# Kernel optimization log

Measured on AMD Instinct MI355X. Metric: run time of the kernel, lower is better.

The kernel has to match this reference:

```python
import jax, jax.numpy as jnp
import numpy as np

N_NODES = 50000
N_EDGES = 600000
HID = 128


def setup_inputs() -> dict:
    key = jax.random.key(0)
    ks = jax.random.split(key, 10)
    s = 1.0 / np.sqrt(HID)
    s2 = 1.0 / np.sqrt(2 * HID)
    return {
        "h": jax.random.normal(ks[0], (N_NODES, HID), dtype=jnp.float32),
        "edge_index": jax.random.randint(ks[1], (2, N_EDGES), 0, N_NODES, dtype=jnp.int64),
        # edge_mlp: Linear(HID,HID) -> ReLU -> Linear(HID,HID); weights stored [in,out]
        "e_w1": jax.random.uniform(ks[2], (HID, HID), jnp.float32, -s, s),
        "e_b1": jax.random.uniform(ks[3], (HID,), jnp.float32, -s, s),
        "e_w2": jax.random.uniform(ks[4], (HID, HID), jnp.float32, -s, s),
        "e_b2": jax.random.uniform(ks[5], (HID,), jnp.float32, -s, s),
        # node_mlp: Linear(2*HID,HID) -> ReLU -> Linear(HID,HID)
        "n_w1": jax.random.uniform(ks[6], (2 * HID, HID), jnp.float32, -s2, s2),
        "n_b1": jax.random.uniform(ks[7], (HID,), jnp.float32, -s2, s2),
        "n_w2": jax.random.uniform(ks[8], (HID, HID), jnp.float32, -s, s),
        "n_b2": jax.random.uniform(ks[9], (HID,), jnp.float32, -s, s),
    }


def reference(h, edge_index, e_w1, e_b1, e_w2, e_b2, n_w1, n_b1, n_w2, n_b2):
    row, col = edge_index[0], edge_index[1]
    # edge model: MLP(h[row] - h[col])  [E, HID]
    diff = h[row] - h[col]
    e = jax.nn.relu(diff @ e_w1 + e_b1) @ e_w2 + e_b2
    # aggregate messages to source nodes (unsorted_segment_sum over row)
    agg = jax.ops.segment_sum(e, row, num_segments=h.shape[0])  # [N, HID]
    # node model: MLP(concat(h, agg))
    z = jnp.concatenate([h, agg], axis=1)  # [N, 2*HID]
    out = jax.nn.relu(z @ n_w1 + n_b1) @ n_w2 + n_b2
    return out
```

## Files before the change

### kernel.cpp

```cpp
#include <hip/hip_runtime.h>
#include <hip/hip_bf16.h>


typedef __attribute__((ext_vector_type(4))) float f32x4;
typedef __attribute__((ext_vector_type(2))) float f32x2;
typedef __attribute__((ext_vector_type(8))) __bf16 bf16x8;
typedef __attribute__((ext_vector_type(4))) short s16x4;
typedef __attribute__((ext_vector_type(8))) unsigned short u16x8;

#define SLOT_CAP 64

__device__ __forceinline__ short f2bf(float f) {
  unsigned x = __float_as_uint(f);
  x = (x + 0x7fffu + ((x >> 16) & 1u)) >> 16;
  return (short)x;
}
__device__ __forceinline__ float bf2f(unsigned short u) {
  return __uint_as_float(((unsigned)u) << 16);
}
__device__ __forceinline__ int swzB(int row, int colByte, int strideB) {
  return row * strideB + (colByte ^ ((row & 7) << 4));
}

__global__ void prep_all(const float* __restrict__ ew1, const float* __restrict__ ew2,
                         const float* __restrict__ eb2, const float* __restrict__ nw1,
                         const float* __restrict__ nw2, short* __restrict__ W1t,
                         short* __restrict__ NW1t, short* __restrict__ NW2t,
                         float* __restrict__ c0, int* __restrict__ deg, int degInt4) {
  int idx = blockIdx.x * 256 + threadIdx.x;
  if (idx < 16384) {
    int n = idx >> 7, k = idx & 127;
    W1t[idx] = f2bf(ew1[k * 128 + n]);
  } else if (idx < 32768) {
    int o = idx - 16384; int n = o >> 7, k = o & 127;
    NW1t[n * 256 + k] = f2bf(nw1[k * 128 + n]);
  } else if (idx < 49152) {
    int o = idx - 32768; int n = o >> 7, k = o & 127;
    NW2t[o] = f2bf(nw2[k * 128 + n]);
  } else if (idx < 65536) {
    int o = idx - 49152; int ocol = o & 127, kt = o >> 7;
    float s = 0.f;
    for (int m = 0; m < 128; ++m) s += ew2[kt * 128 + m] * nw1[(128 + m) * 128 + ocol];
    NW1t[ocol * 256 + 128 + kt] = f2bf(s);
  } else if (idx < 65664) {
    int o = idx - 65536;
    float s = 0.f;
    for (int m = 0; m < 128; ++m) s += eb2[m] * nw1[(128 + m) * 128 + o];
    c0[o] = s;
  } else if (idx < 65664 + degInt4) {
    ((int4*)deg)[idx - 65664] = (int4){0, 0, 0, 0};
  }
}

__global__ __launch_bounds__(256) void g_kernel(
    const float* __restrict__ h, const short* __restrict__ W1t,
    unsigned short* __restrict__ gOut, char* __restrict__ g8, int nN) {
  __shared__ __align__(16) char sW[32768];
  __shared__ __align__(16) char sO[16384];

  const int tid = threadIdx.x;
  const int lane = tid & 63, wv = tid >> 6;
  const int lr = lane & 15, grp = lane >> 4;
  const int nb = blockIdx.x * 64;

#pragma unroll
  for (int i = 0; i < 8; ++i) {
    int c = i * 256 + tid;
    int n = c >> 4, kB = (c & 15) * 16;
    *(int4*)(sW + swzB(n, kB, 256)) = ((const int4*)W1t)[c];
  }
  bf16x8 afr[4];
  {
    int row = nb + wv * 16 + lr;
    int nd = (row < nN) ? row : 0;
    const float* hr = h + (long)nd * 128;
#pragma unroll
    for (int kk = 0; kk < 4; ++kk) {
      int k0 = kk * 32 + grp * 8;
      f32x4 a0 = *(const f32x4*)(hr + k0), a1 = *(const f32x4*)(hr + k0 + 4);
      union { bf16x8 v; short s[8]; } u;
      u.s[0] = f2bf(a0.x); u.s[1] = f2bf(a0.y); u.s[2] = f2bf(a0.z); u.s[3] = f2bf(a0.w);
      u.s[4] = f2bf(a1.x); u.s[5] = f2bf(a1.y); u.s[6] = f2bf(a1.z); u.s[7] = f2bf(a1.w);
      afr[kk] = u.v;
    }
  }
  __syncthreads();

  f32x4 acc[8];
#pragma unroll
  for (int j = 0; j < 8; ++j) acc[j] = (f32x4){0.f, 0.f, 0.f, 0.f};
#pragma unroll
  for (int kk = 0; kk < 4; ++kk) {
    int kB = (kk * 32 + grp * 8) * 2;
#pragma unroll
    for (int j = 0; j < 8; ++j) {
      bf16x8 b = *(const bf16x8*)(sW + swzB(j * 16 + lr, kB, 256));
      acc[j] = __builtin_amdgcn_mfma_f32_16x16x32_bf16(afr[kk], b, acc[j], 0, 0, 0);
    }
  }
#pragma unroll
  for (int j = 0; j < 8; ++j) {
    int col = j * 16 + lr;
#pragma unroll
    for (int r = 0; r < 4; ++r) {
      int row = wv * 16 + grp * 4 + r;
      *(short*)(sO + row * 256 + ((col * 2) ^ ((row & 7) << 4))) = f2bf(acc[j][r]);
    }
  }
  __syncthreads();
#pragma unroll
  for (int i = 0; i < 4; ++i) {
    int c = i * 256 + tid;
    int row = c >> 4;
    int node = nb + row;
    if (node < nN) {
      union { int4 v; unsigned short s[8]; } u;
      u.v = *(const int4*)(sO + row * 256 + (((c & 15) * 16) ^ ((row & 7) << 4)));
      ((int4*)gOut)[node * 16 + (c & 15)] = u.v;
      float f0 = bf2f(u.s[0]), f1 = bf2f(u.s[1]), f2 = bf2f(u.s[2]), f3 = bf2f(u.s[3]);
      float f4 = bf2f(u.s[4]), f5 = bf2f(u.s[5]), f6 = bf2f(u.s[6]), f7 = bf2f(u.s[7]);
      int w0 = __builtin_amdgcn_cvt_pk_fp8_f32(f0, f1, 0, false);
      w0 = __builtin_amdgcn_cvt_pk_fp8_f32(f2, f3, w0, true);
      int w1 = __builtin_amdgcn_cvt_pk_fp8_f32(f4, f5, 0, false);
      w1 = __builtin_amdgcn_cvt_pk_fp8_f32(f6, f7, w1, true);
      int2 pk; pk.x = w0; pk.y = w1;
      *(int2*)(g8 + (long)node * 128 + (c & 15) * 8) = pk;
    }
  }
}

__global__ __launch_bounds__(256) void scatter_kernel(
    const int* __restrict__ ei, int* __restrict__ deg, int* __restrict__ colS, int nE) {
  int e = blockIdx.x * 256 + threadIdx.x;
  if (e < nE) {
    int r = ei[e];
    int pos = atomicAdd(&deg[r], 1);
    if (pos < SLOT_CAP) colS[(long)r * SLOT_CAP + pos] = ei[nE + e];
  }
}

__device__ __forceinline__ void acc16fp8(float* tac, const float* gnb, int4 v, float m) {
  int w[4] = {v.x, v.y, v.z, v.w};
#pragma unroll
  for (int q = 0; q < 4; ++q) {
    f32x2 lo = __builtin_amdgcn_cvt_pk_f32_fp8(w[q], false);
    f32x2 hi = __builtin_amdgcn_cvt_pk_f32_fp8(w[q], true);
    float d0 = gnb[q * 4 + 0] - lo.x;
    float d1 = gnb[q * 4 + 1] - lo.y;
    float d2 = gnb[q * 4 + 2] - hi.x;
    float d3 = gnb[q * 4 + 3] - hi.y;
    tac[q * 4 + 0] += m * (d0 > 0.f ? d0 : 0.f);
    tac[q * 4 + 1] += m * (d1 > 0.f ? d1 : 0.f);
    tac[q * 4 + 2] += m * (d2 > 0.f ? d2 : 0.f);
    tac[q * 4 + 3] += m * (d3 > 0.f ? d3 : 0.f);
  }
}

__global__ __launch_bounds__(256, 4) void agg_node_kernel(
    const float* __restrict__ h, const unsigned short* __restrict__ g,
    const char* __restrict__ g8, const int* __restrict__ deg,
    const int* __restrict__ colS, const float* __restrict__ eb1,
    const float* __restrict__ b1, const float* __restrict__ b2,
    const short* __restrict__ NW1t, const short* __restrict__ NW2t,
    const float* __restrict__ c0, float* __restrict__ out, int nN) {
  __shared__ __align__(16) char sW1[32768];
  __shared__ __align__(16) char sT[8192];

  const int tid = threadIdx.x;
  const int lane = tid & 63, wv = tid >> 6;
  const int lr = lane & 15, grp = lane >> 4;
  const int nb = blockIdx.x * 32;
  const int r0 = (wv >> 1) * 16;
  const int cb = (wv & 1) * 64;

#pragma unroll
  for (int i = 0; i < 8; ++i) {
    int c = i * 256 + tid;
    int n = c >> 4, kB = (c & 15) * 16;
    *(int4*)(sW1 + swzB(n, kB, 256)) = *(const int4*)(NW1t + n * 256 + (c & 15) * 8);
  }

  {
    int gi = tid >> 3;
    int gn = nb + gi;
    bool gok = gn < nN;
    int nd = gok ? gn : 0;
    long rp = (long)nd * SLOT_CAP;
    int dgv = gok ? deg[nd] : 0;
    if (dgv > SLOT_CAP) dgv = SLOT_CAP;
    int d0 = (tid & 7) * 16;

    float gnb[16];
    {
      u16x8 s0 = *(const u16x8*)(g + (long)nd * 128 + d0);
      u16x8 s1 = *(const u16x8*)(g + (long)nd * 128 + d0 + 8);
      f32x4 e0 = *(const f32x4*)(eb1 + d0),     e1 = *(const f32x4*)(eb1 + d0 + 4);
      f32x4 e2 = *(const f32x4*)(eb1 + d0 + 8), e3 = *(const f32x4*)(eb1 + d0 + 12);
#pragma unroll
      for (int j = 0; j < 4; ++j) {
        gnb[j]      = bf2f(s0[j])     + e0[j];
        gnb[4 + j]  = bf2f(s0[4 + j]) + e1[j];
        gnb[8 + j]  = bf2f(s1[j])     + e2[j];
        gnb[12 + j] = bf2f(s1[4 + j]) + e3[j];
      }
    }
    float tac[16];
#pragma unroll
    for (int j = 0; j < 16; ++j) tac[j] = 0.f;

    int cc0, cc1, cc2, cc3;
    cc0 = (0 < dgv) ? colS[rp + 0] : -1;
    cc1 = (1 < dgv) ? colS[rp + 1] : -1;
    cc2 = (2 < dgv) ? colS[rp + 2] : -1;
    cc3 = (3 < dgv) ? colS[rp + 3] : -1;
    for (int i = 0; i < dgv; i += 4) {
      int ii = i + 4;
      int nx0 = (ii + 0 < dgv) ? colS[rp + ii + 0] : -1;
      int nx1 = (ii + 1 < dgv) ? colS[rp + ii + 1] : -1;
      int nx2 = (ii + 2 < dgv) ? colS[rp + ii + 2] : -1;
      int nx3 = (ii + 3 < dgv) ? colS[rp + ii + 3] : -1;
      long r0l = (long)(cc0 < 0 ? 0 : cc0) * 128;
      long r1l = (long)(cc1 < 0 ? 0 : cc1) * 128;
      long r2l = (long)(cc2 < 0 ? 0 : cc2) * 128;
      long r3l = (long)(cc3 < 0 ? 0 : cc3) * 128;
      int4 a0 = *(const int4*)(g8 + r0l + d0);
      int4 a1 = *(const int4*)(g8 + r1l + d0);
      int4 a2 = *(const int4*)(g8 + r2l + d0);
      int4 a3 = *(const int4*)(g8 + r3l + d0);
      float m0 = cc0 < 0 ? 0.f : 1.f, m1 = cc1 < 0 ? 0.f : 1.f;
      float m2 = cc2 < 0 ? 0.f : 1.f, m3 = cc3 < 0 ? 0.f : 1.f;
      acc16fp8(tac, gnb, a0, m0);
      acc16fp8(tac, gnb, a1, m1);
      acc16fp8(tac, gnb, a2, m2);
      acc16fp8(tac, gnb, a3, m3);
      cc0 = nx0; cc1 = nx1; cc2 = nx2; cc3 = nx3;
    }
    union { int4 v; short s[8]; } p0, p1;
#pragma unroll
    for (int j = 0; j < 8; ++j) { p0.s[j] = f2bf(tac[j]); p1.s[j] = f2bf(tac[8 + j]); }
    *(int4*)(sT + swzB(gi, d0 * 2, 256))      = p0.v;
    *(int4*)(sT + swzB(gi, d0 * 2 + 16, 256)) = p1.v;
  }

  const int node = nb + r0 + lr;
  const bool ok = node < nN;
  const int ndd = ok ? node : 0;
  bf16x8 afr[8];
  {
    const float* hr = h + (long)ndd * 128;
#pragma unroll
    for (int kk = 0; kk < 4; ++kk) {
      int k0 = kk * 32 + grp * 8;
      f32x4 a0 = *(const f32x4*)(hr + k0), a1 = *(const f32x4*)(hr + k0 + 4);
      union { bf16x8 v; short s[8]; } u;
      u.s[0] = f2bf(a0.x); u.s[1] = f2bf(a0.y); u.s[2] = f2bf(a0.z); u.s[3] = f2bf(a0.w);
      u.s[4] = f2bf(a1.x); u.s[5] = f2bf(a1.y); u.s[6] = f2bf(a1.z); u.s[7] = f2bf(a1.w);
      if (!ok) u.v = (bf16x8)(__bf16)0.f;
      afr[kk] = u.v;
    }
  }
  __syncthreads();

#pragma unroll
  for (int kk = 0; kk < 4; ++kk) {
    afr[4 + kk] = *(const bf16x8*)(sT + swzB(r0 + lr, (kk * 32 + grp * 8) * 2, 256));
  }

  f32x4 acc[4];
#pragma unroll
  for (int j = 0; j < 4; ++j) acc[j] = (f32x4){0.f, 0.f, 0.f, 0.f};
#pragma unroll
  for (int kk = 0; kk < 4; ++kk) {
    int kB = (kk * 32 + grp * 8) * 2;
#pragma unroll
    for (int j = 0; j < 4; ++j) {
      bf16x8 b = *(const bf16x8*)(sW1 + swzB(cb + j * 16 + lr, kB, 256));
      acc[j] = __builtin_amdgcn_mfma_f32_16x16x32_bf16(afr[kk], b, acc[j], 0, 0, 0);
    }
  }
  __syncthreads();

#pragma unroll
  for (int i = 0; i < 8; ++i) {
    int c = i * 256 + tid;
    int n = c >> 4, kB = (c & 15) * 16;
    *(int4*)(sW1 + swzB(n, kB, 256)) = *(const int4*)(NW1t + n * 256 + 128 + (c & 15) * 8);
  }
  __syncthreads();

#pragma unroll
  for (int kk = 0; kk < 4; ++kk) {
    int kB = (kk * 32 + grp * 8) * 2;
#pragma unroll
    for (int j = 0; j < 4; ++j) {
      bf16x8 b = *(const bf16x8*)(sW1 + swzB(cb + j * 16 + lr, kB, 256));
      acc[j] = __builtin_amdgcn_mfma_f32_16x16x32_bf16(afr[4 + kk], b, acc[j], 0, 0, 0);
    }
  }
  float degs[4];
#pragma unroll
  for (int r = 0; r < 4; ++r) {
    int nn = nb + r0 + grp * 4 + r;
    degs[r] = (float)deg[nn];
  }
#pragma unroll
  for (int j = 0; j < 4; ++j) {
    int col = cb + j * 16 + lr;
    float bv = b1[col];
    float c0v = c0[col];
#pragma unroll
    for (int r = 0; r < 4; ++r) {
      int row = r0 + grp * 4 + r;
      float v = acc[j][r] + bv + degs[r] * c0v;
      v = v > 0.f ? v : 0.f;
      *(short*)(sT + swzB(row, col * 2, 256)) = f2bf(v);
    }
  }
  __syncthreads();

  f32x4 acc2[4];
#pragma unroll
  for (int j = 0; j < 4; ++j) acc2[j] = (f32x4){0.f, 0.f, 0.f, 0.f};
#pragma unroll
  for (int kk = 0; kk < 4; ++kk) {
    int kB = (kk * 32 + grp * 8) * 2;
    bf16x8 a = *(const bf16x8*)(sT + swzB(r0 + lr, kB, 256));
#pragma unroll
    for (int j = 0; j < 4; ++j) {
      bf16x8 b = *(const bf16x8*)(NW2t + (cb + j * 16 + lr) * 128 + kk * 32 + grp * 8);
      acc2[j] = __builtin_amdgcn_mfma_f32_16x16x32_bf16(a, b, acc2[j], 0, 0, 0);
    }
  }
#pragma unroll
  for (int j = 0; j < 4; ++j) {
    int col = cb + j * 16 + lr;
    float bv = b2[col];
#pragma unroll
    for (int r = 0; r < 4; ++r) {
      int nn = nb + r0 + grp * 4 + r;
      if (nn < nN) out[(long)nn * 128 + col] = acc2[j][r] + bv;
    }
  }
}

__global__ void prep_kernel_fb(const float* __restrict__ ew1, const float* __restrict__ ew2,
                               const float* __restrict__ nw1, const float* __restrict__ nw2,
                               short* __restrict__ wsS) {
  int idx = blockIdx.x * 256 + threadIdx.x;
  if (idx < 16384) {
    int n = idx >> 7, k = idx & 127;
    wsS[idx] = f2bf(ew1[k * 128 + n]);
  } else if (idx < 32768) {
    int o = idx - 16384; int n = o >> 7, k = o & 127;
    wsS[idx] = f2bf(ew2[k * 128 + n]);
  } else if (idx < 65536) {
    int o = idx - 32768; int n = o >> 8, k = o & 255;
    wsS[idx] = f2bf(nw1[k * 128 + n]);
  } else if (idx < 81920) {
    int o = idx - 65536; int n = o >> 7, k = o & 127;
    wsS[idx] = f2bf(nw2[k * 128 + n]);
  }
}

__global__ __launch_bounds__(512) void edge_kernel_fb(
    const float* __restrict__ h, const int* __restrict__ ei,
    const float* __restrict__ b1, const float* __restrict__ b2,
    const short* __restrict__ W1t, const short* __restrict__ W2t,
    float* __restrict__ agg, int nE) {
  __shared__ __align__(16) char sW1[32768];
  __shared__ __align__(16) char sW2[32768];
  __shared__ __align__(16) char sT[32768];

  const int tid = threadIdx.x;
  const int lane = tid & 63, wv = tid >> 6;
  const int lr = lane & 15, grp = lane >> 4;
  const int eb = blockIdx.x * 128;
  const int* rowI = ei;
  const int* colI = ei + nE;

#pragma unroll
  for (int i = 0; i < 4; ++i) {
    int c = i * 512 + tid;
    int n = c >> 4, kB = (c & 15) * 16;
    *(int4*)(sW1 + swzB(n, kB, 256)) = ((const int4*)W1t)[c];
    *(int4*)(sW2 + swzB(n, kB, 256)) = ((const int4*)W2t)[c];
  }
  bf16x8 afr[4];
  {
    int slot = eb + wv * 16 + lr;
    int r = 0, cc = 0;
    if (slot < nE) { r = rowI[slot]; cc = colI[slot]; }
    const float* hr = h + (long)r * 128;
    const float* hc = h + (long)cc * 128;
#pragma unroll
    for (int kk = 0; kk < 4; ++kk) {
      int k0 = kk * 32 + grp * 8;
      f32x4 a0 = *(const f32x4*)(hr + k0), a1 = *(const f32x4*)(hr + k0 + 4);
      f32x4 c0_ = *(const f32x4*)(hc + k0), c1 = *(const f32x4*)(hc + k0 + 4);
      union { bf16x8 v; short s[8]; } u;
      u.s[0] = f2bf(a0.x - c0_.x); u.s[1] = f2bf(a0.y - c0_.y);
      u.s[2] = f2bf(a0.z - c0_.z); u.s[3] = f2bf(a0.w - c0_.w);
      u.s[4] = f2bf(a1.x - c1.x); u.s[5] = f2bf(a1.y - c1.y);
      u.s[6] = f2bf(a1.z - c1.z); u.s[7] = f2bf(a1.w - c1.w);
      afr[kk] = u.v;
    }
  }
  __syncthreads();

  f32x4 acc[8];
#pragma unroll
  for (int j = 0; j < 8; ++j) acc[j] = (f32x4){0.f, 0.f, 0.f, 0.f};
#pragma unroll
  for (int kk = 0; kk < 4; ++kk) {
    int kB = (kk * 32 + grp * 8) * 2;
#pragma unroll
    for (int j = 0; j < 8; ++j) {
      bf16x8 b = *(const bf16x8*)(sW1 + swzB(j * 16 + lr, kB, 256));
      acc[j] = __builtin_amdgcn_mfma_f32_16x16x32_bf16(afr[kk], b, acc[j], 0, 0, 0);
    }
  }
#pragma unroll
  for (int j = 0; j < 8; ++j) {
    int col = j * 16 + lr;
    float bv = b1[col];
#pragma unroll
    for (int r = 0; r < 4; ++r) {
      int row = wv * 16 + grp * 4 + r;
      float v = acc[j][r] + bv;
      v = v > 0.f ? v : 0.f;
      *(short*)(sT + swzB(row, col * 2, 256)) = f2bf(v);
    }
  }
  __syncthreads();

  f32x4 acc2[8];
#pragma unroll
  for (int j = 0; j < 8; ++j) acc2[j] = (f32x4){0.f, 0.f, 0.f, 0.f};
#pragma unroll
  for (int kk = 0; kk < 4; ++kk) {
    int kB = (kk * 32 + grp * 8) * 2;
    bf16x8 a = *(const bf16x8*)(sT + swzB(wv * 16 + lr, kB, 256));
#pragma unroll
    for (int j = 0; j < 8; ++j) {
      bf16x8 b = *(const bf16x8*)(sW2 + swzB(j * 16 + lr, kB, 256));
      acc2[j] = __builtin_amdgcn_mfma_f32_16x16x32_bf16(a, b, acc2[j], 0, 0, 0);
    }
  }
  int nd[4]; bool okr[4];
#pragma unroll
  for (int r = 0; r < 4; ++r) {
    int e = eb + wv * 16 + grp * 4 + r;
    okr[r] = e < nE;
    nd[r] = okr[r] ? rowI[e] : 0;
  }
#pragma unroll
  for (int j = 0; j < 8; ++j) {
    int col = j * 16 + lr;
    float bv = b2[col];
#pragma unroll
    for (int r = 0; r < 4; ++r) {
      if (okr[r]) atomicAdd(agg + (long)nd[r] * 128 + col, acc2[j][r] + bv);
    }
  }
}

__global__ __launch_bounds__(512) void node_kernel_fb(
    const float* __restrict__ h, const float* agg,
    const float* __restrict__ b1, const float* __restrict__ b2,
    const short* __restrict__ W1t, const short* __restrict__ W2t,
    float* out, int nN) {
  __shared__ __align__(16) char sZ[32768];
  __shared__ __align__(16) char sW1[65536];
  __shared__ __align__(16) char sW2[32768];
  __shared__ __align__(16) char sT[16384];

  const int tid = threadIdx.x;
  const int lane = tid & 63, wv = tid >> 6;
  const int lr = lane & 15, grp = lane >> 4;
  const int nb = blockIdx.x * 64;

#pragma unroll
  for (int i = 0; i < 8; ++i) {
    int c = i * 512 + tid;
    int n = c >> 5, kB = (c & 31) * 16;
    *(int4*)(sW1 + swzB(n, kB, 512)) = ((const int4*)W1t)[c];
  }
#pragma unroll
  for (int i = 0; i < 4; ++i) {
    int c = i * 512 + tid;
    int n = c >> 4, kB = (c & 15) * 16;
    *(int4*)(sW2 + swzB(n, kB, 256)) = ((const int4*)W2t)[c];
  }
  {
    int i = tid >> 3;
    int node = nb + i;
    bool ok = node < nN;
    int nd = ok ? node : 0;
#pragma unroll
    for (int it = 0; it < 8; ++it) {
      int c4 = (tid & 7) + it * 8;
      int col = c4 * 4;
      f32x4 v;
      if (col < 128) v = *(const f32x4*)(h + (long)nd * 128 + col);
      else           v = *(const f32x4*)(agg + (long)nd * 128 + (col - 128));
      if (!ok) v = (f32x4){0.f, 0.f, 0.f, 0.f};
      s16x4 p;
      p.x = f2bf(v.x); p.y = f2bf(v.y); p.z = f2bf(v.z); p.w = f2bf(v.w);
      *(s16x4*)(sZ + swzB(i, col * 2, 512)) = p;
    }
  }
  __syncthreads();

  const int r0 = (wv >> 1) * 16;
  const int cb = (wv & 1) * 64;
  f32x4 acc[4];
#pragma unroll
  for (int j = 0; j < 4; ++j) acc[j] = (f32x4){0.f, 0.f, 0.f, 0.f};
#pragma unroll
  for (int kk = 0; kk < 8; ++kk) {
    int kB = (kk * 32 + grp * 8) * 2;
    bf16x8 a = *(const bf16x8*)(sZ + swzB(r0 + lr, kB, 512));
#pragma unroll
    for (int j = 0; j < 4; ++j) {
      bf16x8 b = *(const bf16x8*)(sW1 + swzB(cb + j * 16 + lr, kB, 512));
      acc[j] = __builtin_amdgcn_mfma_f32_16x16x32_bf16(a, b, acc[j], 0, 0, 0);
    }
  }
#pragma unroll
  for (int j = 0; j < 4; ++j) {
    int col = cb + j * 16 + lr;
    float bv = b1[col];
#pragma unroll
    for (int r = 0; r < 4; ++r) {
      int row = r0 + grp * 4 + r;
      float v = acc[j][r] + bv;
      v = v > 0.f ? v : 0.f;
      *(short*)(sT + swzB(row, col * 2, 256)) = f2bf(v);
    }
  }
  __syncthreads();

  f32x4 acc2[4];
#pragma unroll
  for (int j = 0; j < 4; ++j) acc2[j] = (f32x4){0.f, 0.f, 0.f, 0.f};
#pragma unroll
  for (int kk = 0; kk < 4; ++kk) {
    int kB = (kk * 32 + grp * 8) * 2;
    bf16x8 a = *(const bf16x8*)(sT + swzB(r0 + lr, kB, 256));
#pragma unroll
    for (int j = 0; j < 4; ++j) {
      bf16x8 b = *(const bf16x8*)(sW2 + swzB(cb + j * 16 + lr, kB, 256));
      acc2[j] = __builtin_amdgcn_mfma_f32_16x16x32_bf16(a, b, acc2[j], 0, 0, 0);
    }
  }
#pragma unroll
  for (int j = 0; j < 4; ++j) {
    int col = cb + j * 16 + lr;
    float bv = b2[col];
#pragma unroll
    for (int r = 0; r < 4; ++r) {
      int node = nb + r0 + grp * 4 + r;
      if (node < nN) out[(long)node * 128 + col] = acc2[j][r] + bv;
    }
  }
}

extern "C" void kernel_launch(void* const* d_in, const int* in_sizes, int n_in,
                              void* d_out, int out_size, void* d_ws, size_t ws_size,
                              hipStream_t stream) {
  const float* h   = (const float*)d_in[0];
  const int*   ei  = (const int*)d_in[1];
  const float* ew1 = (const float*)d_in[2];
  const float* eb1 = (const float*)d_in[3];
  const float* ew2 = (const float*)d_in[4];
  const float* eb2 = (const float*)d_in[5];
  const float* nw1 = (const float*)d_in[6];
  const float* nb1 = (const float*)d_in[7];
  const float* nw2 = (const float*)d_in[8];
  const float* nb2 = (const float*)d_in[9];
  float* out = (float*)d_out;

  const int E = in_sizes[1] / 2;
  const int N = in_sizes[0] / 128;
  const int NP = ((N + 255) / 256) * 256;
  const int degInt4 = NP / 4;

  char* base = (char*)d_ws;
  short* W1t    = (short*)base;
  short* NW1t   = W1t + 16384;
  short* NW2t   = NW1t + 32768;
  float* c0     = (float*)(NW2t + 16384);
  int*   deg    = (int*)(c0 + 128);
  int*   colS   = deg + NP;
  size_t off    = (((size_t)((char*)(colS + (size_t)NP * SLOT_CAP) - base)) + 15) & ~(size_t)15;
  unsigned short* g = (unsigned short*)(base + off);
  char* g8 = (char*)(g + (size_t)NP * 128);
  size_t needed = off + (size_t)NP * 256 + (size_t)NP * 128;

  if (ws_size >= needed) {
    int prepBlocks = (65664 + degInt4 + 255) / 256;
    prep_all<<<prepBlocks, 256, 0, stream>>>(ew1, ew2, eb2, nw1, nw2,
                                             W1t, NW1t, NW2t, c0, deg, degInt4);
    g_kernel<<<(N + 63) / 64, 256, 0, stream>>>(h, W1t, g, g8, N);
    scatter_kernel<<<(E + 255) / 256, 256, 0, stream>>>(ei, deg, colS, E);
    agg_node_kernel<<<(N + 31) / 32, 256, 0, stream>>>(h, g, g8, deg, colS, eb1,
                                                       nb1, nb2, NW1t, NW2t, c0, out, N);
    return;
  }

  short* wsS   = (short*)d_ws;
  short* fW1t  = wsS;
  short* fW2t  = wsS + 16384;
  short* fNW1t = wsS + 32768;
  short* fNW2t = wsS + 65536;
  hipMemsetAsync(d_out, 0, (size_t)out_size * sizeof(float), stream);
  prep_kernel_fb<<<320, 256, 0, stream>>>(ew1, ew2, nw1, nw2, wsS);
  edge_kernel_fb<<<(E + 127) / 128, 512, 0, stream>>>(h, ei, eb1, eb2, fW1t, fW2t, out, E);
  node_kernel_fb<<<(N + 63) / 64, 512, 0, stream>>>(h, out, nb1, nb2, fNW1t, fNW2t, out, N);
}
```

Baseline: 97.64 us.

## Fuse prep, g, scatter and agg-node stages into one cooperative persistent kernel

Replaces the four-kernel sequence with a single cooperative persistent kernel of 512 blocks that uses grid.sync between phases: weight prep, then the g GEMM plus edge scatter, then aggregation with the node MLP. The aim is to remove launch gaps and tail effects between the small kernels. The trade-offs are grid-wide barriers, 72KB of static LDS per block that may limit occupancy, and grid-stride loops that serialise the tiles. The launch falls back to the old multi-kernel path if the cooperative launch fails, and the old atomic fallback path for a small workspace is removed.

```diff
diff --git a/kernel.cpp b/kernel.cpp
--- a/kernel.cpp
+++ b/kernel.cpp
@@ -1,6 +1,9 @@
 #include <hip/hip_runtime.h>
 #include <hip/hip_bf16.h>
-
+#include <hip/hip_cooperative_groups.h>
+
+
+namespace cg = cooperative_groups;
 
 typedef __attribute__((ext_vector_type(4))) float f32x4;
 typedef __attribute__((ext_vector_type(2))) float f32x2;
@@ -20,6 +23,311 @@
 }
 __device__ __forceinline__ int swzB(int row, int colByte, int strideB) {
   return row * strideB + (colByte ^ ((row & 7) << 4));
+}
+
+__device__ __forceinline__ void acc16fp8(float* tac, const float* gnb, int4 v, float m) {
+  int w[4] = {v.x, v.y, v.z, v.w};
+#pragma unroll
+  for (int q = 0; q < 4; ++q) {
+    f32x2 lo = __builtin_amdgcn_cvt_pk_f32_fp8(w[q], false);
+    f32x2 hi = __builtin_amdgcn_cvt_pk_f32_fp8(w[q], true);
+    float d0 = gnb[q * 4 + 0] - lo.x;
+    float d1 = gnb[q * 4 + 1] - lo.y;
+    float d2 = gnb[q * 4 + 2] - hi.x;
+    float d3 = gnb[q * 4 + 3] - hi.y;
+    tac[q * 4 + 0] += m * (d0 > 0.f ? d0 : 0.f);
+    tac[q * 4 + 1] += m * (d1 > 0.f ? d1 : 0.f);
+    tac[q * 4 + 2] += m * (d2 > 0.f ? d2 : 0.f);
+    tac[q * 4 + 3] += m * (d3 > 0.f ? d3 : 0.f);
+  }
+}
+
+__global__ __launch_bounds__(256, 4) void mega_kernel(
+    const float* __restrict__ h, const int* __restrict__ ei,
+    const float* __restrict__ eb1f, const float* __restrict__ nb1f,
+    const float* __restrict__ nb2f, const float* __restrict__ ew1,
+    const float* __restrict__ ew2, const float* __restrict__ eb2,
+    const float* __restrict__ nw1, const float* __restrict__ nw2,
+    short* __restrict__ W1t, short* __restrict__ NW1t, short* __restrict__ NW2t,
+    float* __restrict__ c0, int* __restrict__ deg, int* __restrict__ colS,
+    unsigned short* __restrict__ g, char* __restrict__ g8,
+    float* __restrict__ out, int nN, int nE, int degInt4) {
+  __shared__ __align__(16) char sm[73728];
+  cg::grid_group grid = cg::this_grid();
+  const int tid = threadIdx.x;
+  const int bid = blockIdx.x;
+  const int nBlk = gridDim.x;
+  const int lane = tid & 63, wv = tid >> 6;
+  const int lr = lane & 15, grp = lane >> 4;
+
+  for (int idx = bid * 256 + tid; idx < 65664 + degInt4; idx += nBlk * 256) {
+    if (idx < 16384) {
+      int n = idx >> 7, k = idx & 127;
+      W1t[idx] = f2bf(ew1[k * 128 + n]);
+    } else if (idx < 32768) {
+      int o = idx - 16384; int n = o >> 7, k = o & 127;
+      NW1t[n * 256 + k] = f2bf(nw1[k * 128 + n]);
+    } else if (idx < 49152) {
+      int o = idx - 32768; int n = o >> 7, k = o & 127;
+      NW2t[o] = f2bf(nw2[k * 128 + n]);
+    } else if (idx < 65536) {
+      int o = idx - 49152; int ocol = o & 127, kt = o >> 7;
+      float s = 0.f;
+      for (int m = 0; m < 128; ++m) s += ew2[kt * 128 + m] * nw1[(128 + m) * 128 + ocol];
+      NW1t[ocol * 256 + 128 + kt] = f2bf(s);
+    } else if (idx < 65664) {
+      int o = idx - 65536;
+      float s = 0.f;
+      for (int m = 0; m < 128; ++m) s += eb2[m] * nw1[(128 + m) * 128 + o];
+      c0[o] = s;
+    } else {
+      ((int4*)deg)[idx - 65664] = (int4){0, 0, 0, 0};
+    }
+  }
+  grid.sync();
+
+  {
+    char* sW = sm;
+    char* sO = sm + 32768;
+    for (int i = tid; i < 2048; i += 256) {
+      int n = i >> 4, kB = (i & 15) * 16;
+      *(int4*)(sW + swzB(n, kB, 256)) = ((const int4*)W1t)[i];
+    }
+    __syncthreads();
+    const int gTiles = (nN + 63) >> 6;
+    for (int t = bid; t < gTiles; t += nBlk) {
+      const int nb = t * 64;
+      bf16x8 afr[4];
+      {
+        int row = nb + wv * 16 + lr;
+        int nd = (row < nN) ? row : 0;
+        const float* hr = h + (long)nd * 128;
+#pragma unroll
+        for (int kk = 0; kk < 4; ++kk) {
+          int k0 = kk * 32 + grp * 8;
+          f32x4 a0 = *(const f32x4*)(hr + k0), a1 = *(const f32x4*)(hr + k0 + 4);
+          union { bf16x8 v; short s[8]; } u;
+          u.s[0] = f2bf(a0.x); u.s[1] = f2bf(a0.y); u.s[2] = f2bf(a0.z); u.s[3] = f2bf(a0.w);
+          u.s[4] = f2bf(a1.x); u.s[5] = f2bf(a1.y); u.s[6] = f2bf(a1.z); u.s[7] = f2bf(a1.w);
+          afr[kk] = u.v;
+        }
+      }
+      f32x4 acc[8];
+#pragma unroll
+      for (int j = 0; j < 8; ++j) acc[j] = (f32x4){0.f, 0.f, 0.f, 0.f};
+#pragma unroll
+      for (int kk = 0; kk < 4; ++kk) {
+        int kB = (kk * 32 + grp * 8) * 2;
+#pragma unroll
+        for (int j = 0; j < 8; ++j) {
+          bf16x8 b = *(const bf16x8*)(sW + swzB(j * 16 + lr, kB, 256));
+          acc[j] = __builtin_amdgcn_mfma_f32_16x16x32_bf16(afr[kk], b, acc[j], 0, 0, 0);
+        }
+      }
+      __syncthreads();
+#pragma unroll
+      for (int j = 0; j < 8; ++j) {
+        int col = j * 16 + lr;
+#pragma unroll
+        for (int r = 0; r < 4; ++r) {
+          int row = wv * 16 + grp * 4 + r;
+          *(short*)(sO + row * 256 + ((col * 2) ^ ((row & 7) << 4))) = f2bf(acc[j][r]);
+        }
+      }
+      __syncthreads();
+#pragma unroll
+      for (int i = 0; i < 4; ++i) {
+        int c = i * 256 + tid;
+        int row = c >> 4;
+        int node = nb + row;
+        if (node < nN) {
+          union { int4 v; unsigned short s[8]; } u;
+          u.v = *(const int4*)(sO + row * 256 + (((c & 15) * 16) ^ ((row & 7) << 4)));
+          ((int4*)g)[node * 16 + (c & 15)] = u.v;
+          float f0 = bf2f(u.s[0]), f1 = bf2f(u.s[1]), f2 = bf2f(u.s[2]), f3 = bf2f(u.s[3]);
+          float f4 = bf2f(u.s[4]), f5 = bf2f(u.s[5]), f6 = bf2f(u.s[6]), f7 = bf2f(u.s[7]);
+          int w0 = __builtin_amdgcn_cvt_pk_fp8_f32(f0, f1, 0, false);
+          w0 = __builtin_amdgcn_cvt_pk_fp8_f32(f2, f3, w0, true);
+          int w1 = __builtin_amdgcn_cvt_pk_fp8_f32(f4, f5, 0, false);
+          w1 = __builtin_amdgcn_cvt_pk_fp8_f32(f6, f7, w1, true);
+          int2 pk; pk.x = w0; pk.y = w1;
+          *(int2*)(g8 + (long)node * 128 + (c & 15) * 8) = pk;
+        }
+      }
+    }
+    const int scatChunks = (nE + 255) >> 8;
+    for (int w = bid; w < scatChunks; w += nBlk) {
+      int e = w * 256 + tid;
+      if (e < nE) {
+        int r = ei[e];
+        int pos = atomicAdd(&deg[r], 1);
+        if (pos < SLOT_CAP) colS[(long)r * SLOT_CAP + pos] = ei[nE + e];
+      }
+    }
+  }
+  grid.sync();
+
+  {
+    char* sW1 = sm;
+    char* sT  = sm + 65536;
+    for (int i = tid; i < 4096; i += 256) {
+      int n = i >> 5, kB = (i & 31) * 16;
+      *(int4*)(sW1 + swzB(n, kB, 512)) = ((const int4*)NW1t)[i];
+    }
+    __syncthreads();
+    const int aggTiles = (nN + 31) >> 5;
+    const int r0 = (wv >> 1) * 16;
+    const int cb = (wv & 1) * 64;
+    for (int t = bid; t < aggTiles; t += nBlk) {
+      const int nb = t * 32;
+      {
+        int gi = tid >> 3;
+        int gn = nb + gi;
+        bool gok = gn < nN;
+        int nd = gok ? gn : 0;
+        long rp = (long)nd * SLOT_CAP;
+        int dgv = gok ? deg[nd] : 0;
+        if (dgv > SLOT_CAP) dgv = SLOT_CAP;
+        int d0 = (tid & 7) * 16;
+        float gnb[16];
+        {
+          u16x8 s0 = *(const u16x8*)(g + (long)nd * 128 + d0);
+          u16x8 s1 = *(const u16x8*)(g + (long)nd * 128 + d0 + 8);
+          f32x4 e0 = *(const f32x4*)(eb1f + d0),     e1 = *(const f32x4*)(eb1f + d0 + 4);
+          f32x4 e2 = *(const f32x4*)(eb1f + d0 + 8), e3 = *(const f32x4*)(eb1f + d0 + 12);
+#pragma unroll
+          for (int j = 0; j < 4; ++j) {
+            gnb[j]      = bf2f(s0[j])     + e0[j];
+            gnb[4 + j]  = bf2f(s0[4 + j]) + e1[j];
+            gnb[8 + j]  = bf2f(s1[j])     + e2[j];
+            gnb[12 + j] = bf2f(s1[4 + j]) + e3[j];
+          }
+        }
+        float tac[16];
+#pragma unroll
+        for (int j = 0; j < 16; ++j) tac[j] = 0.f;
+        int cc0 = (0 < dgv) ? colS[rp + 0] : -1;
+        int cc1 = (1 < dgv) ? colS[rp + 1] : -1;
+        int cc2 = (2 < dgv) ? colS[rp + 2] : -1;
+        int cc3 = (3 < dgv) ? colS[rp + 3] : -1;
+        for (int i = 0; i < dgv; i += 4) {
+          int ii = i + 4;
+          int nx0 = (ii + 0 < dgv) ? colS[rp + ii + 0] : -1;
+          int nx1 = (ii + 1 < dgv) ? colS[rp + ii + 1] : -1;
+          int nx2 = (ii + 2 < dgv) ? colS[rp + ii + 2] : -1;
+          int nx3 = (ii + 3 < dgv) ? colS[rp + ii + 3] : -1;
+          long r0l = (long)(cc0 < 0 ? 0 : cc0) * 128;
+          long r1l = (long)(cc1 < 0 ? 0 : cc1) * 128;
+          long r2l = (long)(cc2 < 0 ? 0 : cc2) * 128;
+          long r3l = (long)(cc3 < 0 ? 0 : cc3) * 128;
+          int4 a0 = *(const int4*)(g8 + r0l + d0);
+          int4 a1 = *(const int4*)(g8 + r1l + d0);
+          int4 a2 = *(const int4*)(g8 + r2l + d0);
+          int4 a3 = *(const int4*)(g8 + r3l + d0);
+          float m0 = cc0 < 0 ? 0.f : 1.f, m1 = cc1 < 0 ? 0.f : 1.f;
+          float m2 = cc2 < 0 ? 0.f : 1.f, m3 = cc3 < 0 ? 0.f : 1.f;
+          acc16fp8(tac, gnb, a0, m0);
+          acc16fp8(tac, gnb, a1, m1);
+          acc16fp8(tac, gnb, a2, m2);
+          acc16fp8(tac, gnb, a3, m3);
+          cc0 = nx0; cc1 = nx1; cc2 = nx2; cc3 = nx3;
+        }
+        union { int4 v; short s[8]; } p0, p1;
+#pragma unroll
+        for (int j = 0; j < 8; ++j) { p0.s[j] = f2bf(tac[j]); p1.s[j] = f2bf(tac[8 + j]); }
+        *(int4*)(sT + swzB(gi, d0 * 2, 256))      = p0.v;
+        *(int4*)(sT + swzB(gi, d0 * 2 + 16, 256)) = p1.v;
+      }
+      const int node = nb + r0 + lr;
+      const bool ok = node < nN;
+      const int ndd = ok ? node : 0;
+      bf16x8 afr[8];
+      {
+        const float* hr = h + (long)ndd * 128;
+#pragma unroll
+        for (int kk = 0; kk < 4; ++kk) {
+          int k0 = kk * 32 + grp * 8;
+          f32x4 a0 = *(const f32x4*)(hr + k0), a1 = *(const f32x4*)(hr + k0 + 4);
+          union { bf16x8 v; short s[8]; } u;
+          u.s[0] = f2bf(a0.x); u.s[1] = f2bf(a0.y); u.s[2] = f2bf(a0.z); u.s[3] = f2bf(a0.w);
+          u.s[4] = f2bf(a1.x); u.s[5] = f2bf(a1.y); u.s[6] = f2bf(a1.z); u.s[7] = f2bf(a1.w);
+          if (!ok) u.v = (bf16x8)(__bf16)0.f;
+          afr[kk] = u.v;
+        }
+      }
+      __syncthreads();
+#pragma unroll
+      for (int kk = 0; kk < 4; ++kk) {
+        afr[4 + kk] = *(const bf16x8*)(sT + swzB(r0 + lr, (kk * 32 + grp * 8) * 2, 256));
+      }
+      f32x4 acc[4];
+#pragma unroll
+      for (int j = 0; j < 4; ++j) acc[j] = (f32x4){0.f, 0.f, 0.f, 0.f};
+#pragma unroll
+      for (int kk = 0; kk < 4; ++kk) {
+        int kB = (kk * 32 + grp * 8) * 2;
+#pragma unroll
+        for (int j = 0; j < 4; ++j) {
+          bf16x8 b = *(const bf16x8*)(sW1 + swzB(cb + j * 16 + lr, kB, 512));
+          acc[j] = __builtin_amdgcn_mfma_f32_16x16x32_bf16(afr[kk], b, acc[j], 0, 0, 0);
+        }
+      }
+#pragma unroll
+      for (int kk = 0; kk < 4; ++kk) {
+        int kB = 256 + (kk * 32 + grp * 8) * 2;
+#pragma unroll
+        for (int j = 0; j < 4; ++j) {
+          bf16x8 b = *(const bf16x8*)(sW1 + swzB(cb + j * 16 + lr, kB, 512));
+          acc[j] = __builtin_amdgcn_mfma_f32_16x16x32_bf16(afr[4 + kk], b, acc[j], 0, 0, 0);
+        }
+      }
+      __syncthreads();
+      float degs[4];
+#pragma unroll
+      for (int r = 0; r < 4; ++r) {
+        int nn = nb + r0 + grp * 4 + r;
+        degs[r] = (float)deg[nn];
+      }
+#pragma unroll
+      for (int j = 0; j < 4; ++j) {
+        int col = cb + j * 16 + lr;
+        float bv = nb1f[col];
+        float c0v = c0[col];
+#pragma unroll
+        for (int r = 0; r < 4; ++r) {
+          int row = r0 + grp * 4 + r;
+          float v = acc[j][r] + bv + degs[r] * c0v;
+          v = v > 0.f ? v : 0.f;
+          *(short*)(sT + swzB(row, col * 2, 256)) = f2bf(v);
+        }
+      }
+      __syncthreads();
+      f32x4 acc2[4];
+#pragma unroll
+      for (int j = 0; j < 4; ++j) acc2[j] = (f32x4){0.f, 0.f, 0.f, 0.f};
+#pragma unroll
+      for (int kk = 0; kk < 4; ++kk) {
+        int kB = (kk * 32 + grp * 8) * 2;
+        bf16x8 a = *(const bf16x8*)(sT + swzB(r0 + lr, kB, 256));
+#pragma unroll
+        for (int j = 0; j < 4; ++j) {
+          bf16x8 b = *(const bf16x8*)(NW2t + (cb + j * 16 + lr) * 128 + kk * 32 + grp * 8);
+          acc2[j] = __builtin_amdgcn_mfma_f32_16x16x32_bf16(a, b, acc2[j], 0, 0, 0);
+        }
+      }
+#pragma unroll
+      for (int j = 0; j < 4; ++j) {
+        int col = cb + j * 16 + lr;
+        float bv = nb2f[col];
+#pragma unroll
+        for (int r = 0; r < 4; ++r) {
+          int nn = nb + r0 + grp * 4 + r;
+          if (nn < nN) out[(long)nn * 128 + col] = acc2[j][r] + bv;
+        }
+      }
+      __syncthreads();
+    }
+  }
 }
 
 __global__ void prep_all(const float* __restrict__ ew1, const float* __restrict__ ew2,
@@ -139,23 +447,6 @@
   }
 }
 
-__device__ __forceinline__ void acc16fp8(float* tac, const float* gnb, int4 v, float m) {
-  int w[4] = {v.x, v.y, v.z, v.w};
-#pragma unroll
-  for (int q = 0; q < 4; ++q) {
-    f32x2 lo = __builtin_amdgcn_cvt_pk_f32_fp8(w[q], false);
-    f32x2 hi = __builtin_amdgcn_cvt_pk_f32_fp8(w[q], true);
-    float d0 = gnb[q * 4 + 0] - lo.x;
-    float d1 = gnb[q * 4 + 1] - lo.y;
-    float d2 = gnb[q * 4 + 2] - hi.x;
-    float d3 = gnb[q * 4 + 3] - hi.y;
-    tac[q * 4 + 0] += m * (d0 > 0.f ? d0 : 0.f);
-    tac[q * 4 + 1] += m * (d1 > 0.f ? d1 : 0.f);
-    tac[q * 4 + 2] += m * (d2 > 0.f ? d2 : 0.f);
-    tac[q * 4 + 3] += m * (d3 > 0.f ? d3 : 0.f);
-  }
-}
-
 __global__ __launch_bounds__(256, 4) void agg_node_kernel(
     const float* __restrict__ h, const unsigned short* __restrict__ g,
     const char* __restrict__ g8, const int* __restrict__ deg,
@@ -179,7 +470,6 @@
     int n = c >> 4, kB = (c & 15) * 16;
     *(int4*)(sW1 + swzB(n, kB, 256)) = *(const int4*)(NW1t + n * 256 + (c & 15) * 8);
   }
-
   {
     int gi = tid >> 3;
     int gn = nb + gi;
@@ -208,11 +498,10 @@
 #pragma unroll
     for (int j = 0; j < 16; ++j) tac[j] = 0.f;
 
-    int cc0, cc1, cc2, cc3;
-    cc0 = (0 < dgv) ? colS[rp + 0] : -1;
-    cc1 = (1 < dgv) ? colS[rp + 1] : -1;
-    cc2 = (2 < dgv) ? colS[rp + 2] : -1;
-    cc3 = (3 < dgv) ? colS[rp + 3] : -1;
+    int cc0 = (0 < dgv) ? colS[rp + 0] : -1;
+    int cc1 = (1 < dgv) ? colS[rp + 1] : -1;
+    int cc2 = (2 < dgv) ? colS[rp + 2] : -1;
+    int cc3 = (3 < dgv) ? colS[rp + 3] : -1;
     for (int i = 0; i < dgv; i += 4) {
       int ii = i + 4;
       int nx0 = (ii + 0 < dgv) ? colS[rp + ii + 0] : -1;
@@ -343,228 +632,6 @@
   }
 }
 
-__global__ void prep_kernel_fb(const float* __restrict__ ew1, const float* __restrict__ ew2,
-                               const float* __restrict__ nw1, const float* __restrict__ nw2,
-                               short* __restrict__ wsS) {
-  int idx = blockIdx.x * 256 + threadIdx.x;
-  if (idx < 16384) {
-    int n = idx >> 7, k = idx & 127;
-    wsS[idx] = f2bf(ew1[k * 128 + n]);
-  } else if (idx < 32768) {
-    int o = idx - 16384; int n = o >> 7, k = o & 127;
-    wsS[idx] = f2bf(ew2[k * 128 + n]);
-  } else if (idx < 65536) {
-    int o = idx - 32768; int n = o >> 8, k = o & 255;
-    wsS[idx] = f2bf(nw1[k * 128 + n]);
-  } else if (idx < 81920) {
-    int o = idx - 65536; int n = o >> 7, k = o & 127;
-    wsS[idx] = f2bf(nw2[k * 128 + n]);
-  }
-}
-
-__global__ __launch_bounds__(512) void edge_kernel_fb(
-    const float* __restrict__ h, const int* __restrict__ ei,
-    const float* __restrict__ b1, const float* __restrict__ b2,
-    const short* __restrict__ W1t, const short* __restrict__ W2t,
-    float* __restrict__ agg, int nE) {
-  __shared__ __align__(16) char sW1[32768];
-  __shared__ __align__(16) char sW2[32768];
-  __shared__ __align__(16) char sT[32768];
-
-  const int tid = threadIdx.x;
-  const int lane = tid & 63, wv = tid >> 6;
-  const int lr = lane & 15, grp = lane >> 4;
-  const int eb = blockIdx.x * 128;
-  const int* rowI = ei;
-  const int* colI = ei + nE;
-
-#pragma unroll
-  for (int i = 0; i < 4; ++i) {
-    int c = i * 512 + tid;
-    int n = c >> 4, kB = (c & 15) * 16;
-    *(int4*)(sW1 + swzB(n, kB, 256)) = ((const int4*)W1t)[c];
-    *(int4*)(sW2 + swzB(n, kB, 256)) = ((const int4*)W2t)[c];
-  }
-  bf16x8 afr[4];
-  {
-    int slot = eb + wv * 16 + lr;
-    int r = 0, cc = 0;
-    if (slot < nE) { r = rowI[slot]; cc = colI[slot]; }
-    const float* hr = h + (long)r * 128;
-    const float* hc = h + (long)cc * 128;
-#pragma unroll
-    for (int kk = 0; kk < 4; ++kk) {
-      int k0 = kk * 32 + grp * 8;
-      f32x4 a0 = *(const f32x4*)(hr + k0), a1 = *(const f32x4*)(hr + k0 + 4);
-      f32x4 c0_ = *(const f32x4*)(hc + k0), c1 = *(const f32x4*)(hc + k0 + 4);
-      union { bf16x8 v; short s[8]; } u;
-      u.s[0] = f2bf(a0.x - c0_.x); u.s[1] = f2bf(a0.y - c0_.y);
-      u.s[2] = f2bf(a0.z - c0_.z); u.s[3] = f2bf(a0.w - c0_.w);
-      u.s[4] = f2bf(a1.x - c1.x); u.s[5] = f2bf(a1.y - c1.y);
-      u.s[6] = f2bf(a1.z - c1.z); u.s[7] = f2bf(a1.w - c1.w);
-      afr[kk] = u.v;
-    }
-  }
-  __syncthreads();
-
-  f32x4 acc[8];
-#pragma unroll
-  for (int j = 0; j < 8; ++j) acc[j] = (f32x4){0.f, 0.f, 0.f, 0.f};
-#pragma unroll
-  for (int kk = 0; kk < 4; ++kk) {
-    int kB = (kk * 32 + grp * 8) * 2;
-#pragma unroll
-    for (int j = 0; j < 8; ++j) {
-      bf16x8 b = *(const bf16x8*)(sW1 + swzB(j * 16 + lr, kB, 256));
-      acc[j] = __builtin_amdgcn_mfma_f32_16x16x32_bf16(afr[kk], b, acc[j], 0, 0, 0);
-    }
-  }
-#pragma unroll
-  for (int j = 0; j < 8; ++j) {
-    int col = j * 16 + lr;
-    float bv = b1[col];
-#pragma unroll
-    for (int r = 0; r < 4; ++r) {
-      int row = wv * 16 + grp * 4 + r;
-      float v = acc[j][r] + bv;
-      v = v > 0.f ? v : 0.f;
-      *(short*)(sT + swzB(row, col * 2, 256)) = f2bf(v);
-    }
-  }
-  __syncthreads();
-
-  f32x4 acc2[8];
-#pragma unroll
-  for (int j = 0; j < 8; ++j) acc2[j] = (f32x4){0.f, 0.f, 0.f, 0.f};
-#pragma unroll
-  for (int kk = 0; kk < 4; ++kk) {
-    int kB = (kk * 32 + grp * 8) * 2;
-    bf16x8 a = *(const bf16x8*)(sT + swzB(wv * 16 + lr, kB, 256));
-#pragma unroll
-    for (int j = 0; j < 8; ++j) {
-      bf16x8 b = *(const bf16x8*)(sW2 + swzB(j * 16 + lr, kB, 256));
-      acc2[j] = __builtin_amdgcn_mfma_f32_16x16x32_bf16(a, b, acc2[j], 0, 0, 0);
-    }
-  }
-  int nd[4]; bool okr[4];
-#pragma unroll
-  for (int r = 0; r < 4; ++r) {
-    int e = eb + wv * 16 + grp * 4 + r;
-    okr[r] = e < nE;
-    nd[r] = okr[r] ? rowI[e] : 0;
-  }
-#pragma unroll
-  for (int j = 0; j < 8; ++j) {
-    int col = j * 16 + lr;
-    float bv = b2[col];
-#pragma unroll
-    for (int r = 0; r < 4; ++r) {
-      if (okr[r]) atomicAdd(agg + (long)nd[r] * 128 + col, acc2[j][r] + bv);
-    }
-  }
-}
-
-__global__ __launch_bounds__(512) void node_kernel_fb(
-    const float* __restrict__ h, const float* agg,
-    const float* __restrict__ b1, const float* __restrict__ b2,
-    const short* __restrict__ W1t, const short* __restrict__ W2t,
-    float* out, int nN) {
-  __shared__ __align__(16) char sZ[32768];
-  __shared__ __align__(16) char sW1[65536];
-  __shared__ __align__(16) char sW2[32768];
-  __shared__ __align__(16) char sT[16384];
-
-  const int tid = threadIdx.x;
-  const int lane = tid & 63, wv = tid >> 6;
-  const int lr = lane & 15, grp = lane >> 4;
-  const int nb = blockIdx.x * 64;
-
-#pragma unroll
-  for (int i = 0; i < 8; ++i) {
-    int c = i * 512 + tid;
-    int n = c >> 5, kB = (c & 31) * 16;
-    *(int4*)(sW1 + swzB(n, kB, 512)) = ((const int4*)W1t)[c];
-  }
-#pragma unroll
-  for (int i = 0; i < 4; ++i) {
-    int c = i * 512 + tid;
-    int n = c >> 4, kB = (c & 15) * 16;
-    *(int4*)(sW2 + swzB(n, kB, 256)) = ((const int4*)W2t)[c];
-  }
-  {
-    int i = tid >> 3;
-    int node = nb + i;
-    bool ok = node < nN;
-    int nd = ok ? node : 0;
-#pragma unroll
-    for (int it = 0; it < 8; ++it) {
-      int c4 = (tid & 7) + it * 8;
-      int col = c4 * 4;
-      f32x4 v;
-      if (col < 128) v = *(const f32x4*)(h + (long)nd * 128 + col);
-      else           v = *(const f32x4*)(agg + (long)nd * 128 + (col - 128));
-      if (!ok) v = (f32x4){0.f, 0.f, 0.f, 0.f};
-      s16x4 p;
-      p.x = f2bf(v.x); p.y = f2bf(v.y); p.z = f2bf(v.z); p.w = f2bf(v.w);
-      *(s16x4*)(sZ + swzB(i, col * 2, 512)) = p;
-    }
-  }
-  __syncthreads();
-
-  const int r0 = (wv >> 1) * 16;
-  const int cb = (wv & 1) * 64;
-  f32x4 acc[4];
-#pragma unroll
-  for (int j = 0; j < 4; ++j) acc[j] = (f32x4){0.f, 0.f, 0.f, 0.f};
-#pragma unroll
-  for (int kk = 0; kk < 8; ++kk) {
-    int kB = (kk * 32 + grp * 8) * 2;
-    bf16x8 a = *(const bf16x8*)(sZ + swzB(r0 + lr, kB, 512));
-#pragma unroll
-    for (int j = 0; j < 4; ++j) {
-      bf16x8 b = *(const bf16x8*)(sW1 + swzB(cb + j * 16 + lr, kB, 512));
-      acc[j] = __builtin_amdgcn_mfma_f32_16x16x32_bf16(a, b, acc[j], 0, 0, 0);
-    }
-  }
-#pragma unroll
-  for (int j = 0; j < 4; ++j) {
-    int col = cb + j * 16 + lr;
-    float bv = b1[col];
-#pragma unroll
-    for (int r = 0; r < 4; ++r) {
-      int row = r0 + grp * 4 + r;
-      float v = acc[j][r] + bv;
-      v = v > 0.f ? v : 0.f;
-      *(short*)(sT + swzB(row, col * 2, 256)) = f2bf(v);
-    }
-  }
-  __syncthreads();
-
-  f32x4 acc2[4];
-#pragma unroll
-  for (int j = 0; j < 4; ++j) acc2[j] = (f32x4){0.f, 0.f, 0.f, 0.f};
-#pragma unroll
-  for (int kk = 0; kk < 4; ++kk) {
-    int kB = (kk * 32 + grp * 8) * 2;
-    bf16x8 a = *(const bf16x8*)(sT + swzB(r0 + lr, kB, 256));
-#pragma unroll
-    for (int j = 0; j < 4; ++j) {
-      bf16x8 b = *(const bf16x8*)(sW2 + swzB(cb + j * 16 + lr, kB, 256));
-      acc2[j] = __builtin_amdgcn_mfma_f32_16x16x32_bf16(a, b, acc2[j], 0, 0, 0);
-    }
-  }
-#pragma unroll
-  for (int j = 0; j < 4; ++j) {
-    int col = cb + j * 16 + lr;
-    float bv = b2[col];
-#pragma unroll
-    for (int r = 0; r < 4; ++r) {
-      int node = nb + r0 + grp * 4 + r;
-      if (node < nN) out[(long)node * 128 + col] = acc2[j][r] + bv;
-    }
-  }
-}
-
 extern "C" void kernel_launch(void* const* d_in, const int* in_sizes, int n_in,
                               void* d_out, int out_size, void* d_ws, size_t ws_size,
                               hipStream_t stream) {
@@ -583,7 +650,7 @@
   const int E = in_sizes[1] / 2;
   const int N = in_sizes[0] / 128;
   const int NP = ((N + 255) / 256) * 256;
-  const int degInt4 = NP / 4;
+  int degInt4 = NP / 4;
 
   char* base = (char*)d_ws;
   short* W1t    = (short*)base;
@@ -598,6 +665,16 @@
   size_t needed = off + (size_t)NP * 256 + (size_t)NP * 128;
 
   if (ws_size >= needed) {
+    void* args[] = {(void*)&h, (void*)&ei, (void*)&eb1, (void*)&nb1, (void*)&nb2,
+                    (void*)&ew1, (void*)&ew2, (void*)&eb2, (void*)&nw1, (void*)&nw2,
+                    (void*)&W1t, (void*)&NW1t, (void*)&NW2t, (void*)&c0, (void*)&deg,
+                    (void*)&colS, (void*)&g, (void*)&g8, (void*)&out,
+                    (void*)&N, (void*)&E, (void*)&degInt4};
+    hipError_t err = hipLaunchCooperativeKernel((const void*)mega_kernel,
+                                                dim3(512), dim3(256), args, 0, stream);
+    if (err == hipSuccess) return;
+    (void)hipGetLastError();
+
     int prepBlocks = (65664 + degInt4 + 255) / 256;
     prep_all<<<prepBlocks, 256, 0, stream>>>(ew1, ew2, eb2, nw1, nw2,
                                              W1t, NW1t, NW2t, c0, deg, degInt4);
@@ -605,16 +682,5 @@
     scatter_kernel<<<(E + 255) / 256, 256, 0, stream>>>(ei, deg, colS, E);
     agg_node_kernel<<<(N + 31) / 32, 256, 0, stream>>>(h, g, g8, deg, colS, eb1,
                                                        nb1, nb2, NW1t, NW2t, c0, out, N);
-    return;
-  }
-
-  short* wsS   = (short*)d_ws;
-  short* fW1t  = wsS;
-  short* fW2t  = wsS + 16384;
-  short* fNW1t = wsS + 32768;
-  short* fNW2t = wsS + 65536;
-  hipMemsetAsync(d_out, 0, (size_t)out_size * sizeof(float), stream);
-  prep_kernel_fb<<<320, 256, 0, stream>>>(ew1, ew2, nw1, nw2, wsS);
-  edge_kernel_fb<<<(E + 127) / 128, 512, 0, stream>>>(h, ei, eb1, eb2, fW1t, fW2t, out, E);
-  node_kernel_fb<<<(N + 63) / 64, 512, 0, stream>>>(h, out, nb1, nb2, fNW1t, fNW2t, out, N);
-}
+  }
+}
```

After: 229.8 us. 135% more time.
